# Performance work log

Measured on AMD Instinct MI355X. Metric: run time of the kernel, lower is better.

The kernel has to match this reference:

```python
import jax, jax.numpy as jnp
import numpy as np

N_NODES = 50000
N_EDGES = 1600000
D_IN = 512
D_HEAD = 64
N_HEADS_L1 = 4


def _segment_mean(data, seg_ids, num_segments, counts):
    s = jax.ops.segment_sum(data, seg_ids, num_segments=num_segments)
    denom = jnp.maximum(counts, 1.0)
    return jnp.where(counts[:, None] > 0, s / denom[:, None], 0.0)


def setup_inputs() -> dict:
    key = jax.random.key(0)
    k1, k2, k3, k4 = jax.random.split(key, 4)
    node_features = jax.random.normal(k1, (N_NODES, D_IN), dtype=jnp.float32)
    edge_index = jax.random.randint(k2, (2, N_EDGES), 0, N_NODES, dtype=jnp.int32)
    W1 = jax.random.normal(k3, (N_HEADS_L1, D_IN, D_HEAD), dtype=jnp.float32) * (1.0 / np.sqrt(D_IN))
    W2 = jax.random.normal(k4, (N_HEADS_L1 * D_HEAD, D_HEAD), dtype=jnp.float32) * (1.0 / np.sqrt(N_HEADS_L1 * D_HEAD))
    return {"node_features": node_features, "edge_index": edge_index, "W1": W1, "W2": W2}


def reference(node_features, edge_index, W1, W2):
    n = node_features.shape[0]
    src = edge_index[0]  # segment ids (destination of aggregation in TF code)
    dst = edge_index[1]  # gathered neighbors
    counts = jax.ops.segment_sum(jnp.ones_like(src, dtype=node_features.dtype), src, num_segments=n)

    # Layer 1: 4 heads, Dense(64, no bias) -> gather(dst) -> unsorted_segment_mean(src) -> concat -> elu
    head_outs = []
    for i in range(N_HEADS_L1):
        t = node_features @ W1[i]                 # (N, 64)
        agg = _segment_mean(t[dst], src, n, counts)  # (N, 64)
        head_outs.append(agg)
    h = jax.nn.elu(jnp.concatenate(head_outs, axis=-1))  # (N, 256)

    # Layer 2: 1 head, linear activation
    t2 = h @ W2                                   # (N, 64)
    out = _segment_mean(t2[dst], src, n, counts)  # (N, 64)
    return out
```

## Files before the change

kernel.cpp:

```cpp
#include <hip/hip_runtime.h>
#include <hip/hip_bf16.h>
#include <stdint.h>

#define N_NODES 50000
#define N_EDGES 1600000
#define D_IN    512
#define D_H1    256
#define D_OUT   64

#define NBUK    196
#define MAXB    9216
#define EPB     4096
#define NPB     391
#define SLOT    96

#define NR      50001
#define ZROW    50000

typedef __attribute__((ext_vector_type(8))) short  short8;
typedef __attribute__((ext_vector_type(4))) float  f32x4;
typedef __attribute__((ext_vector_type(2))) float  f32x2;
typedef __attribute__((ext_vector_type(4))) unsigned int u32x4;
typedef __attribute__((ext_vector_type(2))) unsigned int u32x2;

typedef __attribute__((address_space(1))) void GASV;
typedef __attribute__((address_space(3))) void LASV;

static __device__ __forceinline__ unsigned short f2bf(float f) {
    union { float f; unsigned int u; } c; c.f = f;
    unsigned int u = c.u;
    return (unsigned short)((u + 0x7FFFu + ((u >> 16) & 1u)) >> 16);
}
static __device__ __forceinline__ unsigned int cvtpk(float a, float b) {
    unsigned int r;
    asm("v_cvt_pk_bf16_f32 %0, %1, %2" : "=v"(r) : "v"(a), "v"(b));
    return r;
}
static __device__ __forceinline__ unsigned short f2bf1(float f) {
    return (unsigned short)cvtpk(f, f);
}
static __device__ __forceinline__ float uasf(unsigned int u) {
    union { unsigned int u; float f; } c; c.u = u; return c.f;
}
static __device__ __forceinline__ void glds16(const unsigned int* g, unsigned int* l) {
    __builtin_amdgcn_global_load_lds((GASV*)g, (LASV*)l, 16, 0, 0);
}


__global__ __launch_bounds__(256) void part_kernel(const int* __restrict__ src,
                                                   const int* __restrict__ dst,
                                                   int* __restrict__ gcnt,
                                                   unsigned int* __restrict__ gbuk) {
    __shared__ int hist[NBUK];
    __shared__ int lofs[NBUK];
    __shared__ int gbase[NBUK];
    __shared__ int sbuf[256];
    __shared__ unsigned int sorted[EPB];
    __shared__ unsigned char bid[EPB];

    const int t  = threadIdx.x;
    const int e0 = blockIdx.x * EPB;
    int ec = N_EDGES - e0; if (ec > EPB) ec = EPB;

    for (int i = t; i < NBUK; i += 256) hist[i] = 0;
    __syncthreads();

    unsigned int rec[16];
    int bb[16], idx[16];
#pragma unroll
    for (int j = 0; j < 16; ++j) {
        int i = j * 256 + t;
        if (i < ec) {
            int s = src[e0 + i], d = dst[e0 + i];
            int b = s >> 8;
            rec[j] = ((unsigned int)(s & 255) << 16) | (unsigned int)d;
            bb[j]  = b;
            idx[j] = atomicAdd(&hist[b], 1);
        } else bb[j] = -1;
    }
    __syncthreads();

    int v = (t < NBUK) ? hist[t] : 0;
    sbuf[t] = v;
    __syncthreads();
#pragma unroll
    for (int off = 1; off < 256; off <<= 1) {
        int x = (t >= off) ? sbuf[t - off] : 0;
        __syncthreads();
        sbuf[t] += x;
        __syncthreads();
    }
    if (t < NBUK) {
        lofs[t]  = sbuf[t] - v;
        gbase[t] = atomicAdd(&gcnt[t], v);
    }
    __syncthreads();

#pragma unroll
    for (int j = 0; j < 16; ++j) {
        if (bb[j] >= 0) {
            int p = lofs[bb[j]] + idx[j];
            sorted[p] = rec[j];
            bid[p] = (unsigned char)bb[j];
        }
    }
    __syncthreads();

    for (int i = t; i < ec; i += 256) {
        int b = bid[i];
        int p = gbase[b] + (i - lofs[b]);
        gbuk[(size_t)b * MAXB + p] = sorted[i];
    }
}


__global__ __launch_bounds__(256) void sort_kernel(const int* __restrict__ gcnt,
                                                   const unsigned int* __restrict__ gbuk,
                                                   unsigned short* __restrict__ sdst,
                                                   int* __restrict__ deg) {
    __shared__ int hist[256];
    __shared__ int nofs[256];
    __shared__ int sbuf[256];
    __shared__ unsigned short list[MAXB];

    const int t = threadIdx.x;
    const int b = blockIdx.x;
    const int cnt = gcnt[b];
    const unsigned int* buk = gbuk + (size_t)b * MAXB;

    hist[t] = 0;
    __syncthreads();
    for (int i = t; i < cnt; i += 256)
        atomicAdd(&hist[buk[i] >> 16], 1);
    __syncthreads();

    int v = hist[t];
    sbuf[t] = v;
    __syncthreads();
#pragma unroll
    for (int off = 1; off < 256; off <<= 1) {
        int x = (t >= off) ? sbuf[t - off] : 0;
        __syncthreads();
        sbuf[t] += x;
        __syncthreads();
    }
    nofs[t] = sbuf[t] - v;
    const int n = b * 256 + t;
    if (n < N_NODES) deg[n] = v;
    __syncthreads();

    for (int i = t; i < cnt; i += 256) {
        unsigned int r = buk[i];
        int p = atomicAdd(&nofs[r >> 16], 1);
        list[p] = (unsigned short)(r & 0xffffu);
    }
    __syncthreads();

    for (int base = 0; base < 256; base += 32) {
        int node = base + (t >> 3);
        int l8   = t & 7;
        int vv   = hist[node];
        int beg  = nofs[node] - vv;
        int n2   = b * 256 + node;
        if (n2 < N_NODES) {
            int words = ((vv + 7) & ~7) >> 1;
            unsigned int* out32 = (unsigned int*)(sdst + (size_t)n2 * SLOT);
            for (int j2 = l8; j2 < words; j2 += 8) {
                unsigned int lo = (2 * j2     < vv) ? list[beg + 2 * j2]     : (unsigned int)ZROW;
                unsigned int hi = (2 * j2 + 1 < vv) ? list[beg + 2 * j2 + 1] : (unsigned int)ZROW;
                out32[j2] = lo | (hi << 16);
            }
        }
    }
}


__global__ void convw_kernel(const float* __restrict__ W1, const float* __restrict__ W2,
                             unsigned short* __restrict__ Bt1, unsigned short* __restrict__ Bt2,
                             unsigned short* __restrict__ t1, unsigned short* __restrict__ t2) {
    int i = blockIdx.x * 256 + threadIdx.x;
    if (i < 4 * 512 * 64) {
        int h = i >> 15;
        int k = (i >> 6) & 511;
        int j = i & 63;
        Bt1[(h * 64 + j) * 512 + k] = f2bf(W1[i]);
    } else if (i < 4 * 512 * 64 + 256 * 64) {
        int r = i - 4 * 512 * 64;
        int k = r >> 6;
        int n = r & 63;
        Bt2[n * 256 + k] = f2bf(W2[r]);
    } else {
        int r = i - (4 * 512 * 64 + 256 * 64);
        if (r < 256) {
            t1[(size_t)ZROW * 256 + r] = 0;
        } else if (r < 256 + 64) {
            t2[(size_t)ZROW * 64 + (r - 256)] = 0;
        }
    }
}


__global__ __launch_bounds__(512) void gemm1_kernel(const float* __restrict__ A,
                                                    const unsigned short* __restrict__ Bt,
                                                    unsigned short* __restrict__ C) {
    constexpr int BM = 128, BK = 32, LDK = 40, K = D_IN, M = N_NODES;
    __shared__ unsigned short As[BM * LDK];
    __shared__ unsigned short Bs[256 * LDK];

    const int tid  = threadIdx.x;
    const int lane = tid & 63;
    const int w    = tid >> 6;
    const int wm   = (w >> 2) * 64;
    const int wn   = (w & 3) * 64;
    const int quad = lane >> 4;
    const int l15  = lane & 15;
    const int bm   = blockIdx.x;

    f32x4 acc[4][4];
#pragma unroll
    for (int mi = 0; mi < 4; ++mi)
#pragma unroll
        for (int ni = 0; ni < 4; ++ni)
            acc[mi][ni] = (f32x4){0.f, 0.f, 0.f, 0.f};

    const int r0 = tid >> 2;
    const int f8 = tid & 3;

    for (int k0 = 0; k0 < K; k0 += BK) {
        {
            int grow = bm * BM + r0;
            if (grow >= M) grow = M - 1;
            const float* ap = A + (size_t)grow * K + k0 + f8 * 8;
            f32x4 v0 = *(const f32x4*)ap;
            f32x4 v1 = *(const f32x4*)(ap + 4);
            u32x4 pk;
            pk[0] = cvtpk(v0[0], v0[1]);
            pk[1] = cvtpk(v0[2], v0[3]);
            pk[2] = cvtpk(v1[0], v1[1]);
            pk[3] = cvtpk(v1[2], v1[3]);
            *(u32x4*)&As[r0 * LDK + f8 * 8] = pk;
        }
        {
#pragma unroll
            for (int p = 0; p < 2; ++p) {
                int row = p * 128 + r0;
                u32x4 v = *(const u32x4*)(Bt + (size_t)row * K + k0 + f8 * 8);
                *(u32x4*)&Bs[row * LDK + f8 * 8] = v;
            }
        }
        __syncthreads();

        short8 af[4], bfr[4];
#pragma unroll
        for (int mi = 0; mi < 4; ++mi)
            af[mi] = *(const short8*)&As[(wm + mi * 16 + l15) * LDK + quad * 8];
#pragma unroll
        for (int ni = 0; ni < 4; ++ni)
            bfr[ni] = *(const short8*)&Bs[(wn + ni * 16 + l15) * LDK + quad * 8];
#pragma unroll
        for (int mi = 0; mi < 4; ++mi)
#pragma unroll
            for (int ni = 0; ni < 4; ++ni)
                acc[mi][ni] = __builtin_amdgcn_mfma_f32_16x16x32_bf16(af[mi], bfr[ni], acc[mi][ni], 0, 0, 0);
        __syncthreads();
    }

#pragma unroll
    for (int mi = 0; mi < 4; ++mi) {
        int row0 = bm * BM + wm + mi * 16 + quad * 4;
#pragma unroll
        for (int ni = 0; ni < 4; ++ni) {
            int col = wn + ni * 16 + l15;
#pragma unroll
            for (int r = 0; r < 4; ++r) {
                int row = row0 + r;
                if (row < M) C[(size_t)row * 256 + col] = f2bf1(acc[mi][ni][r]);
            }
        }
    }
}


__global__ __launch_bounds__(256) void aggf_kernel(const unsigned short* __restrict__ t1,
                                                   const int* __restrict__ deg,
                                                   const unsigned short* __restrict__ sdst,
                                                   const unsigned short* __restrict__ Bt2,
                                                   unsigned short* __restrict__ t2) {
    __shared__ __align__(16) unsigned int ring[4][2][1024];
    __shared__ __align__(16) unsigned short h_lds[16][264];

    const int w    = __builtin_amdgcn_readfirstlane(threadIdx.x >> 6);
    const int lane = threadIdx.x & 63;
    const int s0b  = blockIdx.x * 16;
    const int s0   = s0b + w * 4;
    const unsigned int* tb32 = (const unsigned int*)t1;
    const unsigned int loff = ((unsigned)(lane & 31)) << 2;

    const int end0 = deg[s0 + 0], end1 = deg[s0 + 1], end2 = deg[s0 + 2], end3 = deg[s0 + 3];
    const int elv0 = sdst[(size_t)(s0 + 0) * SLOT + lane];
    const int elv1 = sdst[(size_t)(s0 + 1) * SLOT + lane];
    const int elv2 = sdst[(size_t)(s0 + 2) * SLOT + lane];
    const int elv3 = sdst[(size_t)(s0 + 3) * SLOT + lane];
    asm volatile("" :: "v"(end0), "v"(end1), "v"(end2), "v"(end3),
                       "v"(elv0), "v"(elv1), "v"(elv2), "v"(elv3));

#define AGGF_ISSUE(ELV, C, B)                                                           \
    {                                                                                   \
        int q  = ((C) << 3) + (lane >> 5);                                              \
        int ra = __shfl(ELV, q);                                                        \
        int rb_ = __shfl(ELV, q + 2);                                                   \
        int rc = __shfl(ELV, q + 4);                                                    \
        int rd = __shfl(ELV, q + 6);                                                    \
        unsigned int* dp = &ring[w][B][0];                                              \
        glds16(tb32 + (unsigned)ra  * 128u + loff, dp);                                 \
        glds16(tb32 + (unsigned)rb_ * 128u + loff, dp + 256);                           \
        glds16(tb32 + (unsigned)rc  * 128u + loff, dp + 512);                           \
        glds16(tb32 + (unsigned)rd  * 128u + loff, dp + 768);                           \
    }

#define AGGF_CONSUME(B)                                                                 \
    {                                                                                   \
        const unsigned int* rbp = &ring[w][B][lane << 1];                               \
        _Pragma("unroll")                                                               \
        for (int r = 0; r < 8; ++r) {                                                   \
            u32x2 v = *(const u32x2*)(rbp + (r << 7));                                  \
            a0 += uasf(v[0] << 16); a1 += uasf(v[0] & 0xffff0000u);                     \
            a2 += uasf(v[1] << 16); a3 += uasf(v[1] & 0xffff0000u);                     \
        }                                                                               \
    }

#define AGGF_NODE(J)                                                                    \
    {                                                                                   \
        const int end = end##J;                                                         \
        const int nch = ((end + 7) & ~7) >> 3;                                          \
        float a0 = 0.f, a1 = 0.f, a2 = 0.f, a3 = 0.f;                                   \
        if (nch > 0) {                                                                  \
            AGGF_ISSUE(elv##J, 0, 0);                                                   \
            for (int c = 1; c < nch; ++c) {                                             \
                AGGF_ISSUE(elv##J, c, c & 1);                                           \
                asm volatile("s_waitcnt vmcnt(4)" ::: "memory");                        \
                __builtin_amdgcn_sched_barrier(0);                                      \
                AGGF_CONSUME((c - 1) & 1);                                              \
            }                                                                           \
            asm volatile("s_waitcnt vmcnt(0)" ::: "memory");                            \
            __builtin_amdgcn_sched_barrier(0);                                          \
            AGGF_CONSUME((nch - 1) & 1);                                                \
        }                                                                               \
        float iv = (end > 0) ? (1.0f / (float)end) : 0.f;                               \
        float m0 = a0 * iv, m1 = a1 * iv, m2 = a2 * iv, m3 = a3 * iv;                   \
        m0 = (m0 > 0.f) ? m0 : (__expf(m0) - 1.f);                                      \
        m1 = (m1 > 0.f) ? m1 : (__expf(m1) - 1.f);                                      \
        m2 = (m2 > 0.f) ? m2 : (__expf(m2) - 1.f);                                      \
        m3 = (m3 > 0.f) ? m3 : (__expf(m3) - 1.f);                                      \
        u32x2 hw;                                                                       \
        hw[0] = cvtpk(m0, m1);                                                          \
        hw[1] = cvtpk(m2, m3);                                                          \
        *(u32x2*)&h_lds[(w << 2) + J][lane << 2] = hw;                                  \
    }

    AGGF_NODE(0);
    AGGF_NODE(1);
    AGGF_NODE(2);
    AGGF_NODE(3);

    __syncthreads();

    {
        const int l15 = lane & 15, quad = lane >> 4;
        f32x4 acc = (f32x4){0.f, 0.f, 0.f, 0.f};
#pragma unroll
        for (int st = 0; st < 8; ++st) {
            short8 afr = *(const short8*)&h_lds[l15][st * 32 + quad * 8];
            short8 bfr = *(const short8*)(Bt2 + (size_t)(w * 16 + l15) * 256 + st * 32 + quad * 8);
            acc = __builtin_amdgcn_mfma_f32_16x16x32_bf16(afr, bfr, acc, 0, 0, 0);
        }
#pragma unroll
        for (int r = 0; r < 4; ++r)
            t2[(size_t)(s0b + quad * 4 + r) * 64 + w * 16 + l15] = f2bf1(acc[r]);
    }
}


__global__ __launch_bounds__(256) void agg2_kernel(const unsigned short* __restrict__ t2,
                                                   const int* __restrict__ deg,
                                                   const unsigned short* __restrict__ sdst,
                                                   float* __restrict__ out) {
    __shared__ __align__(16) unsigned int ring[4][2][256];

    const int w    = __builtin_amdgcn_readfirstlane(threadIdx.x >> 6);
    const int lane = threadIdx.x & 63;
    const int s0   = blockIdx.x * 16 + w * 4;
    const unsigned int* tb32 = (const unsigned int*)t2;
    const unsigned int loff = ((unsigned)(lane & 7)) << 2;

    const int end0 = deg[s0 + 0], end1 = deg[s0 + 1], end2 = deg[s0 + 2], end3 = deg[s0 + 3];
    const int elv0 = sdst[(size_t)(s0 + 0) * SLOT + lane];
    const int elv1 = sdst[(size_t)(s0 + 1) * SLOT + lane];
    const int elv2 = sdst[(size_t)(s0 + 2) * SLOT + lane];
    const int elv3 = sdst[(size_t)(s0 + 3) * SLOT + lane];
    asm volatile("" :: "v"(end0), "v"(end1), "v"(end2), "v"(end3),
                       "v"(elv0), "v"(elv1), "v"(elv2), "v"(elv3));

#define AGG2_ISSUE(ELV, D, B)                                                           \
    {                                                                                   \
        int r = __shfl(ELV, ((D) << 3) + (lane >> 3));                                  \
        glds16(tb32 + (unsigned)r * 32u + loff, &ring[w][B][0]);                        \
    }

#define AGG2_CONSUME(B)                                                                 \
    {                                                                                   \
        const unsigned int* rbp = &ring[w][B][lane & 31];                               \
        _Pragma("unroll")                                                               \
        for (int i = 0; i < 4; ++i) {                                                   \
            unsigned int v = rbp[(((i << 1) + (lane >> 5)) << 5)];                      \
            a0 += uasf(v << 16); a1 += uasf(v & 0xffff0000u);                           \
        }                                                                               \
    }

#define AGG2_NODE(J)                                                                    \
    {                                                                                   \
        const int end = end##J;                                                         \
        const int nch = ((end + 7) & ~7) >> 3;                                          \
        float a0 = 0.f, a1 = 0.f;                                                       \
        if (nch > 0) {                                                                  \
            AGG2_ISSUE(elv##J, 0, 0);                                                   \
            for (int d = 1; d < nch; ++d) {                                             \
                AGG2_ISSUE(elv##J, d, d & 1);                                           \
                asm volatile("s_waitcnt vmcnt(1)" ::: "memory");                        \
                __builtin_amdgcn_sched_barrier(0);                                      \
                AGG2_CONSUME((d - 1) & 1);                                              \
            }                                                                           \
            asm volatile("s_waitcnt vmcnt(0)" ::: "memory");                            \
            __builtin_amdgcn_sched_barrier(0);                                          \
            AGG2_CONSUME((nch - 1) & 1);                                                \
        }                                                                               \
        a0 += __shfl_xor(a0, 32);                                                       \
        a1 += __shfl_xor(a1, 32);                                                       \
        if (lane < 32) {                                                                \
            float iv = (end > 0) ? (1.0f / (float)end) : 0.f;                           \
            f32x2 rr; rr.x = a0 * iv; rr.y = a1 * iv;                                   \
            *(f32x2*)(out + (size_t)(s0 + J) * D_OUT + (lane & 31) * 2) = rr;           \
        }                                                                               \
    }

    AGG2_NODE(0);
    AGG2_NODE(1);
    AGG2_NODE(2);
    AGG2_NODE(3);
}


extern "C" void kernel_launch(void* const* d_in, const int* in_sizes, int n_in,
                              void* d_out, int out_size, void* d_ws, size_t ws_size,
                              hipStream_t stream) {
    const float* X  = (const float*)d_in[0];
    const int*   ei = (const int*)d_in[1];
    const float* W1 = (const float*)d_in[2];
    const float* W2 = (const float*)d_in[3];
    const int* src = ei;
    const int* dst = ei + N_EDGES;

    char* ws = (char*)d_ws;
    size_t off = 0;
    auto alloc = [&](size_t bytes) {
        off = (off + 255) & ~(size_t)255;
        void* p = ws + off;
        off += bytes;
        return p;
    };
    int*          gcnt = (int*)alloc((size_t)NBUK * 4);
    unsigned int* gbuk = (unsigned int*)alloc((size_t)NBUK * MAXB * 4);
    unsigned short* sdst = (unsigned short*)alloc(((size_t)N_NODES * SLOT + 64) * 2);
    int*          deg  = (int*)alloc((size_t)N_NODES * 4);
    unsigned short* Bt1 = (unsigned short*)alloc((size_t)D_H1 * D_IN * 2);
    unsigned short* Bt2 = (unsigned short*)alloc((size_t)D_OUT * D_H1 * 2);
    unsigned short* t1  = (unsigned short*)alloc((size_t)NR * D_H1 * 2);
    unsigned short* t2  = (unsigned short*)alloc((size_t)NR * D_OUT * 2);

    hipMemsetAsync(gcnt, 0, (size_t)NBUK * 4, stream);

    part_kernel<<<NPB, 256, 0, stream>>>(src, dst, gcnt, gbuk);
    sort_kernel<<<NBUK, 256, 0, stream>>>(gcnt, gbuk, sdst, deg);
    convw_kernel<<<(4 * 512 * 64 + 256 * 64 + 256 + 64 + 255) / 256, 256, 0, stream>>>(
        W1, W2, Bt1, Bt2, t1, t2);

    gemm1_kernel<<<(N_NODES + 127) / 128, 512, 0, stream>>>(X, Bt1, t1);
    aggf_kernel<<<N_NODES / 16, 256, 0, stream>>>(t1, deg, sdst, Bt2, t2);
    agg2_kernel<<<N_NODES / 16, 256, 0, stream>>>(t2, deg, sdst, (float*)d_out);
}
```

Measured before the change: 351.7 us.

## Trim tail gathers in layer-1 aggregation and pipeline layer-2 gathers across nodes

In the layer-1 aggregation, the last partial chunk of each node now issues only the row loads it needs, and the wait counts match the number of loads actually issued. This cuts wasted gather traffic on the zero-padding rows. In the layer-2 aggregation, all neighbor rows of a node are issued at once into a much larger per-wave LDS buffer. Loads for the next node overlap with summing the current one, replacing the per-chunk double buffer. The larger LDS footprint (64KB per block) may limit occupancy, and a node with more than 64 neighbors relies on the buffer still fitting.

```diff
diff --git a/kernel.cpp b/kernel.cpp
--- a/kernel.cpp
+++ b/kernel.cpp
@@ -44,6 +44,22 @@
 }
 static __device__ __forceinline__ void glds16(const unsigned int* g, unsigned int* l) {
     __builtin_amdgcn_global_load_lds((GASV*)g, (LASV*)l, 16, 0, 0);
+}
+
+static __device__ __forceinline__ void waitvm(int n) {
+    switch (n) {
+    case 0: asm volatile("s_waitcnt vmcnt(0)" ::: "memory"); break;
+    case 1: asm volatile("s_waitcnt vmcnt(1)" ::: "memory"); break;
+    case 2: asm volatile("s_waitcnt vmcnt(2)" ::: "memory"); break;
+    case 3: asm volatile("s_waitcnt vmcnt(3)" ::: "memory"); break;
+    case 4: asm volatile("s_waitcnt vmcnt(4)" ::: "memory"); break;
+    case 5: asm volatile("s_waitcnt vmcnt(5)" ::: "memory"); break;
+    case 6: asm volatile("s_waitcnt vmcnt(6)" ::: "memory"); break;
+    case 7: asm volatile("s_waitcnt vmcnt(7)" ::: "memory"); break;
+    case 8: asm volatile("s_waitcnt vmcnt(8)" ::: "memory"); break;
+    default: asm volatile("s_waitcnt vmcnt(9)" ::: "memory"); break;
+    }
+    __builtin_amdgcn_sched_barrier(0);
 }
 
 
@@ -304,7 +320,7 @@
     asm volatile("" :: "v"(end0), "v"(end1), "v"(end2), "v"(end3),
                        "v"(elv0), "v"(elv1), "v"(elv2), "v"(elv3));
 
-#define AGGF_ISSUE(ELV, C, B)                                                           \
+#define AGGF_ISSUE_FULL(ELV, C, B)                                                      \
     {                                                                                   \
         int q  = ((C) << 3) + (lane >> 5);                                              \
         int ra = __shfl(ELV, q);                                                        \
@@ -318,11 +334,18 @@
         glds16(tb32 + (unsigned)rd  * 128u + loff, dp + 768);                           \
     }
 
-#define AGGF_CONSUME(B)                                                                 \
+#define AGGF_ISSUE_TAIL(ELV, C, B, TQ)                                                  \
+    {                                                                                   \
+        for (int d = 0; d < (TQ); ++d) {                                                \
+            int r = __shfl(ELV, ((C) << 3) + (d << 1) + (lane >> 5));                   \
+            glds16(tb32 + (unsigned)r * 128u + loff, &ring[w][B][d << 8]);              \
+        }                                                                               \
+    }
+
+#define AGGF_CONSUME(B, RC)                                                             \
     {                                                                                   \
         const unsigned int* rbp = &ring[w][B][lane << 1];                               \
-        _Pragma("unroll")                                                               \
-        for (int r = 0; r < 8; ++r) {                                                   \
+        for (int r = 0; r < (RC); ++r) {                                                \
             u32x2 v = *(const u32x2*)(rbp + (r << 7));                                  \
             a0 += uasf(v[0] << 16); a1 += uasf(v[0] & 0xffff0000u);                     \
             a2 += uasf(v[1] << 16); a3 += uasf(v[1] & 0xffff0000u);                     \
@@ -331,20 +354,24 @@
 
 #define AGGF_NODE(J)                                                                    \
     {                                                                                   \
-        const int end = end##J;                                                         \
-        const int nch = ((end + 7) & ~7) >> 3;                                          \
+        const int end   = end##J;                                                       \
+        const int rows2 = (end + 1) >> 1;                       \
+        const int nfull = rows2 >> 2;                            \
+        const int tq2   = rows2 & 3;                               \
+        const int ncht  = nfull + (tq2 ? 1 : 0);                                        \
         float a0 = 0.f, a1 = 0.f, a2 = 0.f, a3 = 0.f;                                   \
-        if (nch > 0) {                                                                  \
-            AGGF_ISSUE(elv##J, 0, 0);                                                   \
-            for (int c = 1; c < nch; ++c) {                                             \
-                AGGF_ISSUE(elv##J, c, c & 1);                                           \
-                asm volatile("s_waitcnt vmcnt(4)" ::: "memory");                        \
-                __builtin_amdgcn_sched_barrier(0);                                      \
-                AGGF_CONSUME((c - 1) & 1);                                              \
+        if (ncht > 0) {                                                                 \
+            if (nfull > 0) { AGGF_ISSUE_FULL(elv##J, 0, 0); }                           \
+            else           { AGGF_ISSUE_TAIL(elv##J, 0, 0, tq2); }                      \
+            for (int c = 1; c < ncht; ++c) {                                            \
+                int nc;                                                                 \
+                if (c < nfull) { AGGF_ISSUE_FULL(elv##J, c, c & 1); nc = 4; }           \
+                else           { AGGF_ISSUE_TAIL(elv##J, c, c & 1, tq2); nc = tq2; }    \
+                waitvm(nc);                                                             \
+                AGGF_CONSUME((c - 1) & 1, 8);                                           \
             }                                                                           \
-            asm volatile("s_waitcnt vmcnt(0)" ::: "memory");                            \
-            __builtin_amdgcn_sched_barrier(0);                                          \
-            AGGF_CONSUME((nch - 1) & 1);                                                \
+            waitvm(0);                                                                  \
+            AGGF_CONSUME((ncht - 1) & 1, (tq2 ? (tq2 << 1) : 8));                       \
         }                                                                               \
         float iv = (end > 0) ? (1.0f / (float)end) : 0.f;                               \
         float m0 = a0 * iv, m1 = a1 * iv, m2 = a2 * iv, m3 = a3 * iv;                   \
@@ -385,7 +412,7 @@
                                                    const int* __restrict__ deg,
                                                    const unsigned short* __restrict__ sdst,
                                                    float* __restrict__ out) {
-    __shared__ __align__(16) unsigned int ring[4][2][256];
+    __shared__ __align__(16) unsigned int ring2[4][2][2048];
 
     const int w    = __builtin_amdgcn_readfirstlane(threadIdx.x >> 6);
     const int lane = threadIdx.x & 63;
@@ -401,52 +428,46 @@
     asm volatile("" :: "v"(end0), "v"(end1), "v"(end2), "v"(end3),
                        "v"(elv0), "v"(elv1), "v"(elv2), "v"(elv3));
 
-#define AGG2_ISSUE(ELV, D, B)                                                           \
+#define A2_ISSUE(J, B, NJ)                                                              \
+    int NJ;                                                                             \
     {                                                                                   \
-        int r = __shfl(ELV, ((D) << 3) + (lane >> 3));                                  \
-        glds16(tb32 + (unsigned)r * 32u + loff, &ring[w][B][0]);                        \
-    }
-
-#define AGG2_CONSUME(B)                                                                 \
-    {                                                                                   \
-        const unsigned int* rbp = &ring[w][B][lane & 31];                               \
-        _Pragma("unroll")                                                               \
-        for (int i = 0; i < 4; ++i) {                                                   \
-            unsigned int v = rbp[(((i << 1) + (lane >> 5)) << 5)];                      \
-            a0 += uasf(v << 16); a1 += uasf(v & 0xffff0000u);                           \
+        const int nd = ((end##J + 7) & ~7) >> 3;                         \
+        for (int d = 0; d < nd; ++d) {                                                  \
+            int r = __shfl(elv##J, (d << 3) + (lane >> 3));                             \
+            glds16(tb32 + (unsigned)r * 32u + loff, &ring2[w][B][d << 8]);              \
         }                                                                               \
-    }
-
-#define AGG2_NODE(J)                                                                    \
+        NJ = nd;                                                                        \
+    }
+
+#define A2_CONSUME(J, B)                                                                \
     {                                                                                   \
         const int end = end##J;                                                         \
-        const int nch = ((end + 7) & ~7) >> 3;                                          \
+        const int nr  = (end + 7) & ~7;                                                 \
+        const int c   = lane & 31;                                                      \
         float a0 = 0.f, a1 = 0.f;                                                       \
-        if (nch > 0) {                                                                  \
-            AGG2_ISSUE(elv##J, 0, 0);                                                   \
-            for (int d = 1; d < nch; ++d) {                                             \
-                AGG2_ISSUE(elv##J, d, d & 1);                                           \
-                asm volatile("s_waitcnt vmcnt(1)" ::: "memory");                        \
-                __builtin_amdgcn_sched_barrier(0);                                      \
-                AGG2_CONSUME((d - 1) & 1);                                              \
-            }                                                                           \
-            asm volatile("s_waitcnt vmcnt(0)" ::: "memory");                            \
-            __builtin_amdgcn_sched_barrier(0);                                          \
-            AGG2_CONSUME((nch - 1) & 1);                                                \
+        for (int r = lane >> 5; r < nr; r += 2) {                                       \
+            unsigned int v = ring2[w][B][(((r >> 3) << 8) | ((r & 7) << 5)) + c];       \
+            a0 += uasf(v << 16); a1 += uasf(v & 0xffff0000u);                           \
         }                                                                               \
         a0 += __shfl_xor(a0, 32);                                                       \
         a1 += __shfl_xor(a1, 32);                                                       \
         if (lane < 32) {                                                                \
             float iv = (end > 0) ? (1.0f / (float)end) : 0.f;                           \
             f32x2 rr; rr.x = a0 * iv; rr.y = a1 * iv;                                   \
-            *(f32x2*)(out + (size_t)(s0 + J) * D_OUT + (lane & 31) * 2) = rr;           \
+            *(f32x2*)(out + (size_t)(s0 + J) * D_OUT + c * 2) = rr;                     \
         }                                                                               \
-    }
-
-    AGG2_NODE(0);
-    AGG2_NODE(1);
-    AGG2_NODE(2);
-    AGG2_NODE(3);
+        __builtin_amdgcn_sched_barrier(0);                                              \
+    }
+
+    A2_ISSUE(0, 0, n0i);
+    A2_ISSUE(1, 1, n1i); waitvm(n1i);
+    A2_CONSUME(0, 0);
+    A2_ISSUE(2, 0, n2i); waitvm(n2i + 1);
+    A2_CONSUME(1, 1);
+    A2_ISSUE(3, 1, n3i); waitvm(n3i + 1);
+    A2_CONSUME(2, 0);
+    waitvm(1);
+    A2_CONSUME(3, 1);
 }
 
 
```

Result: slower. 374.2 us (+6.4%).
